# Kernel optimization log

Hardware: AMD Instinct MI355X
Metric: run time of the kernel (lower is better)

Reference implementation:

```python
import jax, jax.numpy as jnp
import numpy as np
import math

B, H, W = 16, 48, 48
D_MODEL, D_EXP, D_INNER, N, DR, K = 96, 192, 192, 16, 6, 4
L = H * W

def depthwise_conv(x, w, b, pad):
    # x: NHWC, w: (kh,kw,1,C) depthwise kernel
    C = x.shape[-1]
    y = jax.lax.conv_general_dilated(x, w, (1, 1), [(pad, pad), (pad, pad)],
        dimension_numbers=('NHWC', 'HWIO', 'NHWC'), feature_group_count=C)
    return y + b

def bn(x, g, be, m, v):
    return (x - m) * jax.lax.rsqrt(v + 1e-5) * g + be

def cross_scan(x):  # (B,C,H,W) -> (B,K,C,L): row-major, col-major, and their reverses
    x0 = x.reshape(B, -1, L)
    x1 = jnp.swapaxes(x, 2, 3).reshape(B, -1, L)
    return jnp.stack([x0, x1, x0[..., ::-1], x1[..., ::-1]], axis=1)

def cross_merge(ys):  # (B,K,C,L) -> (B,C,L)
    y0 = ys[:, 0] + ys[:, 2][..., ::-1]
    y1 = ys[:, 1] + ys[:, 3][..., ::-1]
    y1 = jnp.swapaxes(y1.reshape(B, -1, W, H), 2, 3).reshape(B, -1, L)
    return y0 + y1

def selective_scan(u, delta, A, Bm, Cm):
    # u, delta: (B,K,D,L); A: (K,D,N); Bm, Cm: (B,K,N,L)
    h0 = jnp.zeros((B, K, D_INNER, N), dtype=u.dtype)
    def step(h, inp):
        d_t, u_t, B_t, C_t = inp  # (B,K,D),(B,K,D),(B,K,N),(B,K,N)
        h = h * jnp.exp(d_t[..., None] * A) + (d_t * u_t)[..., None] * B_t[:, :, None, :]
        return h, jnp.einsum('bkdn,bkn->bkd', h, C_t)
    seq = (jnp.moveaxis(delta, -1, 0), jnp.moveaxis(u, -1, 0),
           jnp.moveaxis(Bm, -1, 0), jnp.moveaxis(Cm, -1, 0))
    _, ys = jax.lax.scan(step, h0, seq)
    return jnp.moveaxis(ys, 0, -1)  # (B,K,D,L)

def setup_inputs():
    key = jax.random.key(0)
    ks = jax.random.split(key, 30)
    rn = lambda i, s, sc=0.05: jax.random.normal(ks[i], s, jnp.float32) * sc
    # faithful dt bias init: inverse-softplus of delta ~ logU[1e-3, 1e-1]
    dlt = jnp.exp(jax.random.uniform(ks[0], (K, D_INNER)) * (math.log(0.1) - math.log(0.001)) + math.log(0.001))
    return {
        'x': jax.random.normal(ks[1], (B, H, W, D_MODEL), jnp.float32),
        'in_proj_w': rn(2, (2 * D_EXP, D_MODEL)),
        'conv_w': rn(3, (3, 3, 1, D_EXP), 0.2),
        'conv_b': rn(4, (D_EXP,)),
        'x_proj_w': rn(5, (K, DR + 2 * N, D_INNER)),
        'dt_proj_w': rn(6, (K, D_INNER, DR), DR ** -0.5),
        'dt_proj_b': dlt + jnp.log(-jnp.expm1(-dlt)),
        'A_log': jnp.tile(jnp.log(jnp.arange(1, N + 1, dtype=jnp.float32)), (K, D_INNER, 1)),
        'Ds': jnp.ones((K, D_INNER), jnp.float32),
        'out_proj_w': rn(7, (D_MODEL, D_EXP)),
        'e1_w': rn(8, (2 * D_EXP, D_EXP)), 'e1_b': rn(9, (2 * D_EXP,)),
        'bn1_g': jnp.ones((2 * D_EXP,), jnp.float32), 'bn1_b': rn(10, (2 * D_EXP,)),
        'bn1_m': rn(11, (2 * D_EXP,)), 'bn1_v': jnp.ones((2 * D_EXP,), jnp.float32),
        'e2_w': rn(12, (3, 3, 1, 2 * D_EXP), 0.2), 'e2_b': rn(13, (2 * D_EXP,)),
        'bn2_g': jnp.ones((2 * D_EXP,), jnp.float32), 'bn2_b': rn(14, (2 * D_EXP,)),
        'bn2_m': rn(15, (2 * D_EXP,)), 'bn2_v': jnp.ones((2 * D_EXP,), jnp.float32),
        'e3_w': rn(16, (D_EXP // 2, 2 * D_EXP)), 'e3_b': rn(17, (D_EXP // 2,)),
        'se1_w': rn(18, (D_EXP // 4, D_EXP // 2)), 'se1_b': rn(19, (D_EXP // 4,)),
        'se2_w': rn(20, (D_EXP // 2, D_EXP // 4)), 'se2_b': rn(21, (D_EXP // 2,)),
    }

def reference(x, in_proj_w, conv_w, conv_b, x_proj_w, dt_proj_w, dt_proj_b, A_log, Ds,
              out_proj_w, e1_w, e1_b, bn1_g, bn1_b, bn1_m, bn1_v, e2_w, e2_b,
              bn2_g, bn2_b, bn2_m, bn2_v, e3_w, e3_b, se1_w, se1_b, se2_w, se2_b):
    # in-projection -> (x, gate z)
    xz = jnp.einsum('bhwd,ed->bhwe', x, in_proj_w)
    xc, z = jnp.split(xz, 2, axis=-1)
    # depthwise conv + SiLU
    xc = jax.nn.silu(depthwise_conv(xc, conv_w, conv_b, 1))     # (B,H,W,C)
    xs = cross_scan(jnp.transpose(xc, (0, 3, 1, 2)))            # (B,K,C,L)
    # per-direction projections to (delta_rank, B, C)
    dbl = jnp.einsum('bkdl,kcd->bkcl', xs, x_proj_w)
    dts, Bm, Cm = dbl[:, :, :DR], dbl[:, :, DR:DR + N], dbl[:, :, DR + N:]
    delta = jax.nn.softplus(jnp.einsum('bkrl,kdr->bkdl', dts, dt_proj_w) + dt_proj_b[None, :, :, None])
    ys = selective_scan(xs, delta, -jnp.exp(A_log), Bm, Cm)
    ys = ys + Ds[None, :, :, None] * xs                          # D skip
    y = jnp.transpose(cross_merge(ys).reshape(B, -1, H, W), (0, 2, 3, 1))  # (B,H,W,C)
    y = y * jax.nn.silu(z)                                       # gate
    out = jnp.einsum('bhwe,de->bhwd', y, out_proj_w)
    # EFFN branch (1x1 -> BN/ReLU -> dw3x3 -> BN/ReLU -> 1x1 -> SE)
    t = jax.nn.relu(bn(jnp.einsum('bhwc,oc->bhwo', y, e1_w) + e1_b, bn1_g, bn1_b, bn1_m, bn1_v))
    t = jax.nn.relu(bn(depthwise_conv(t, e2_w, e2_b, 1), bn2_g, bn2_b, bn2_m, bn2_v))
    t = jnp.einsum('bhwc,oc->bhwo', t, e3_w) + e3_b              # (B,H,W,D_MODEL)
    s = jnp.mean(t, axis=(1, 2))
    s = jax.nn.sigmoid(jax.nn.relu(s @ se1_w.T + se1_b) @ se2_w.T + se2_b)
    return out + t * s[:, None, None, :]
```

## Files before the change

### kernel.cpp

```cpp
#include <hip/hip_runtime.h>
#include <cstddef>

#define BB   16
#define HH   48
#define WW   48
#define LL   2304
#define MTOT 36864
#define DM   96
#define DE   192
#define NS   16
#define KD   4
#define DRK  6
#define CPROJ 152
#define DSTRIDE 40
#define SCH  36
#define LC   64

typedef unsigned short u16;
typedef __attribute__((ext_vector_type(8))) short  short8;
typedef __attribute__((ext_vector_type(4))) float  f4;
typedef __attribute__((ext_vector_type(2))) float  f2;
typedef __attribute__((ext_vector_type(4))) unsigned short us4;

__device__ __forceinline__ float bf2f(u16 u) {
  union { unsigned int i; float f; } c; c.i = ((unsigned int)u) << 16; return c.f;
}
__device__ __forceinline__ u16 f2bf(float f) {
  union { float f; unsigned int i; } c; c.f = f;
  unsigned int r = c.i + 0x7FFFu + ((c.i >> 16) & 1u);
  return (u16)(r >> 16);
}

__global__ __launch_bounds__(256) void cast_f2b(
    const float* __restrict__ src, u16* __restrict__ dst, int n4)
{
  int i = blockIdx.x * 256 + threadIdx.x;
  if (i >= n4) return;
  float4 v = ((const float4*)src)[i];
  us4 o;
  o.x = f2bf(v.x); o.y = f2bf(v.y); o.z = f2bf(v.z); o.w = f2bf(v.w);
  ((us4*)dst)[i] = o;
}

__global__ __launch_bounds__(256) void cast_weights(
    const float* __restrict__ w0, const float* __restrict__ w1,
    const float* __restrict__ w2, const float* __restrict__ w3,
    const float* __restrict__ w4, u16* __restrict__ dst)
{
  int i = blockIdx.x * 256 + threadIdx.x;
  if (i >= 195072) return;
  float v;
  if      (i <  36864) v = w0[i];
  else if (i <  66048) v = w1[i - 36864];
  else if (i <  84480) v = w2[i - 66048];
  else if (i < 158208) v = w3[i - 84480];
  else                 v = w4[i - 158208];
  dst[i] = f2bf(v);
}

template<int MODE, int K>
__global__ __launch_bounds__(256) void gemm_mfma(
    const u16* __restrict__ A, const u16* __restrict__ Wb,
    float* __restrict__ outF, u16* __restrict__ outB,
    const float* __restrict__ q0, const float* __restrict__ q1,
    const float* __restrict__ q2, const float* __restrict__ q3,
    const float* __restrict__ q4, int N)
{
  constexpr int KP = K + 8;
  constexpr int KC = K / 8;
  __shared__ u16 Bs[64 * KP];

  const int tid = threadIdx.x;
  const int m0 = blockIdx.x * 256;
  const int n0 = blockIdx.y * 64;

  for (int i = tid; i < 64 * KC; i += 256) {
    int row = i / KC, ch = i - row * KC;
    short8 v = {0, 0, 0, 0, 0, 0, 0, 0};
    if (n0 + row < N)
      v = *(const short8*)(Wb + (size_t)(n0 + row) * K + ch * 8);
    *(short8*)(&Bs[row * KP + ch * 8]) = v;
  }
  __syncthreads();

  const int lane = tid & 63;
  const int wv = tid >> 6;
  const int l15 = lane & 15;
  const int q8 = (lane >> 4) << 3;

  f4 acc[4][4];
#pragma unroll
  for (int mi = 0; mi < 4; ++mi)
#pragma unroll
    for (int ni = 0; ni < 4; ++ni)
      acc[mi][ni] = (f4){0.f, 0.f, 0.f, 0.f};

  const u16* Ap = A + (size_t)(m0 + wv * 64 + l15) * K + q8;

  for (int k0 = 0; k0 < K; k0 += 32) {
    short8 af[4], bf[4];
#pragma unroll
    for (int mi = 0; mi < 4; ++mi)
      af[mi] = *(const short8*)(Ap + (size_t)(mi * 16) * K + k0);
#pragma unroll
    for (int ni = 0; ni < 4; ++ni)
      bf[ni] = *(const short8*)(&Bs[(ni * 16 + l15) * KP + k0 + q8]);
#pragma unroll
    for (int mi = 0; mi < 4; ++mi)
#pragma unroll
      for (int ni = 0; ni < 4; ++ni)
        acc[mi][ni] = __builtin_amdgcn_mfma_f32_16x16x32_bf16(
            af[mi], bf[ni], acc[mi][ni], 0, 0, 0);
  }

#pragma unroll
  for (int mi = 0; mi < 4; ++mi) {
    int rbase = m0 + wv * 64 + mi * 16 + ((lane >> 4) << 2);
#pragma unroll
    for (int ni = 0; ni < 4; ++ni) {
      int col = n0 + ni * 16 + l15;
#pragma unroll
      for (int r = 0; r < 4; ++r) {
        int row = rbase + r;
        float v = acc[mi][ni][r];
        if (MODE == 0) {
          if (col < DE) outB[(size_t)row * DE + col] = f2bf(v);
          else          outF[(size_t)row * DE + (col - DE)] = v / (1.f + __expf(-v));
        } else if (MODE == 1) {
          if (col < N) outF[(size_t)row * N + col] = v;
        } else if (MODE == 2) {
          float t = (v + q0[col] - q3[col]) * q1[col] * rsqrtf(q4[col] + 1e-5f) + q2[col];
          outB[(size_t)row * 384 + col] = f2bf(fmaxf(t, 0.f));
        } else if (MODE == 3) {
          if (col < N) outF[(size_t)row * N + col] = v + q0[col];
        } else {
          if (col < CPROJ) {
            int kk = col / 38, cc = col - kk * 38;
            outF[((size_t)kk * MTOT + row) * DSTRIDE + cc] = v;
          }
        }
      }
    }
  }
}

template<int MODE, int C>
__global__ __launch_bounds__(256) void dwconv_b(
    const u16* __restrict__ in, const float* __restrict__ w9,
    const float* __restrict__ bias,
    const float* __restrict__ bg, const float* __restrict__ bbe,
    const float* __restrict__ bm, const float* __restrict__ bv,
    u16* __restrict__ out)
{
  constexpr int C4 = C / 4;
  int idx = blockIdx.x * 256 + threadIdx.x;
  if (idx >= MTOT * C4) return;
  int c4 = idx % C4;
  int pos = idx / C4;
  int hw = pos % LL;
  int b = pos / LL;
  int h = hw / WW, w = hw - (hw / WW) * WW;
  int c = c4 * 4;
  f4 acc = (f4){0.f, 0.f, 0.f, 0.f};
#pragma unroll
  for (int dh = -1; dh <= 1; ++dh) {
    int h2 = h + dh;
    if ((unsigned)h2 >= (unsigned)HH) continue;
#pragma unroll
    for (int dw = -1; dw <= 1; ++dw) {
      int w2 = w + dw;
      if ((unsigned)w2 >= (unsigned)WW) continue;
      const u16* ip = in + ((size_t)(b * LL + h2 * WW + w2)) * C + c;
      us4 uv = *(const us4*)ip;
      float4 wvv = *(const float4*)(w9 + ((dh + 1) * 3 + (dw + 1)) * C + c);
      acc[0] = fmaf(bf2f(uv.x), wvv.x, acc[0]);
      acc[1] = fmaf(bf2f(uv.y), wvv.y, acc[1]);
      acc[2] = fmaf(bf2f(uv.z), wvv.z, acc[2]);
      acc[3] = fmaf(bf2f(uv.w), wvv.w, acc[3]);
    }
  }
  float4 bi = *(const float4*)(bias + c);
  float vv[4] = {acc[0] + bi.x, acc[1] + bi.y, acc[2] + bi.z, acc[3] + bi.w};
  us4 o;
  if (MODE == 0) {
#pragma unroll
    for (int j = 0; j < 4; ++j) vv[j] = vv[j] / (1.f + __expf(-vv[j]));
  } else {
    float4 g = *(const float4*)(bg + c);
    float4 be = *(const float4*)(bbe + c);
    float4 mm = *(const float4*)(bm + c);
    float4 va = *(const float4*)(bv + c);
    float gg[4] = {g.x, g.y, g.z, g.w}, bb[4] = {be.x, be.y, be.z, be.w};
    float m4[4] = {mm.x, mm.y, mm.z, mm.w}, v4[4] = {va.x, va.y, va.z, va.w};
#pragma unroll
    for (int j = 0; j < 4; ++j)
      vv[j] = fmaxf((vv[j] - m4[j]) * gg[j] * rsqrtf(v4[j] + 1e-5f) + bb[j], 0.f);
  }
  o.x = f2bf(vv[0]); o.y = f2bf(vv[1]); o.z = f2bf(vv[2]); o.w = f2bf(vv[3]);
  *(us4*)(out + (size_t)pos * C + c) = o;
}

struct PosIter {
  int k, pos, hq, wq;
  __device__ __forceinline__ void init(int kk, int i0) {
    k = kk;
    if (k == 0) { pos = i0; }
    else if (k == 2) { pos = LL - 1 - i0; }
    else {
      int j = (k == 1) ? i0 : (LL - 1 - i0);
      wq = j / HH; hq = j - wq * HH;
      pos = hq * WW + wq;
    }
  }
  __device__ __forceinline__ void next() {
    if (k == 0) { ++pos; }
    else if (k == 2) { --pos; }
    else if (k == 1) {
      ++hq; pos += WW;
      if (hq == HH) { hq = 0; ++wq; pos = wq; }
    } else {
      --hq; pos -= WW;
      if (hq < 0) { hq = HH - 1; --wq; pos = hq * WW + wq; }
    }
  }
};

__global__ __launch_bounds__(192) void scan_part1(
    const u16* __restrict__ xc, const float* __restrict__ dbl,
    const float* __restrict__ dtw, const float* __restrict__ dtb,
    const float* __restrict__ Alog,
    float* __restrict__ hloc, float* __restrict__ sd)
{
  int blk = blockIdx.x;
  int s = blk % SCH;
  int bk = blk / SCH;
  int k = bk & 3;
  int b = bk >> 2;
  int d = threadIdx.x;
  float wr[DRK];
#pragma unroll
  for (int r = 0; r < DRK; ++r) wr[r] = dtw[(k * DE + d) * DRK + r];
  float bias = dtb[k * DE + d];
  float a0 = -__expf(Alog[(k * DE + d) * NS]);
  f2 h2[8];
#pragma unroll
  for (int j = 0; j < 8; ++j) h2[j] = (f2){0.f, 0.f};
  float sumd = 0.f;
  const u16* xcb = xc + (size_t)b * LL * DE + d;
  const float* dpr = dbl + ((size_t)k * MTOT + (size_t)b * LL) * DSTRIDE;
  PosIter it; it.init(k, s * LC);
#pragma unroll 1
  for (int ii = 0; ii < LC; ++ii) {
    const float4* dp4 = (const float4*)(dpr + (size_t)it.pos * DSTRIDE);
    float4 rr[6];
#pragma unroll
    for (int t = 0; t < 6; ++t) rr[t] = dp4[t];
    const float* rf = (const float*)rr;
    float g = bias;
#pragma unroll
    for (int r = 0; r < DRK; ++r) g = fmaf(rf[r], wr[r], g);
    float e = __expf(g);
    float delta = (g > 20.f) ? g : __logf(1.f + e);
    float p = __expf(delta * a0);
    sumd += delta;
    float du = delta * bf2f(xcb[(size_t)it.pos * DE]);
    f2 du2 = (f2){du, du};
    f2 qq = (f2){p, p * p};
    f2 p2 = (f2){qq.y, qq.y};
#pragma unroll
    for (int j = 0; j < 8; ++j) {
      f2 bv = (f2){rf[6 + 2 * j], rf[7 + 2 * j]};
      h2[j] = h2[j] * qq + du2 * bv;
      qq = qq * p2;
    }
    it.next();
  }
  size_t base = ((size_t)blk * NS) * DE + d;
#pragma unroll
  for (int j = 0; j < 8; ++j) {
    hloc[base + (size_t)(2 * j) * DE] = h2[j].x;
    hloc[base + (size_t)(2 * j + 1) * DE] = h2[j].y;
  }
  sd[(size_t)blk * DE + d] = sumd;
}

__global__ __launch_bounds__(192) void scan_part2(
    const float* __restrict__ hloc, const float* __restrict__ sd,
    const float* __restrict__ Alog, float* __restrict__ hin)
{
  int bk = blockIdx.x;
  int k = bk & 3;
  int d = threadIdx.x;
  float a0 = -__expf(Alog[(k * DE + d) * NS]);
  float h[NS];
#pragma unroll
  for (int n = 0; n < NS; ++n) h[n] = 0.f;
  for (int s = 0; s < SCH; ++s) {
    size_t base = ((size_t)(bk * SCH + s) * NS) * DE + d;
#pragma unroll
    for (int n = 0; n < NS; ++n) hin[base + (size_t)n * DE] = h[n];
    float qs = __expf(sd[(size_t)(bk * SCH + s) * DE + d] * a0);
    float q = 1.f;
#pragma unroll
    for (int n = 0; n < NS; ++n) {
      q *= qs;
      h[n] = fmaf(h[n], q, hloc[base + (size_t)n * DE]);
    }
  }
}

__global__ __launch_bounds__(192) void scan_part3(
    const u16* __restrict__ xc, const float* __restrict__ dbl,
    const float* __restrict__ dtw, const float* __restrict__ dtb,
    const float* __restrict__ Alog, const float* __restrict__ Dsw,
    const float* __restrict__ hin, float* __restrict__ ym)
{
  int blk = blockIdx.x;
  int s = blk % SCH;
  int bk = blk / SCH;
  int k = bk & 3;
  int b = bk >> 2;
  int d = threadIdx.x;
  float wr[DRK];
#pragma unroll
  for (int r = 0; r < DRK; ++r) wr[r] = dtw[(k * DE + d) * DRK + r];
  float bias = dtb[k * DE + d];
  float a0 = -__expf(Alog[(k * DE + d) * NS]);
  float dsv = Dsw[k * DE + d];
  f2 h2[8];
  size_t hbase = ((size_t)blk * NS) * DE + d;
#pragma unroll
  for (int j = 0; j < 8; ++j) {
    h2[j].x = hin[hbase + (size_t)(2 * j) * DE];
    h2[j].y = hin[hbase + (size_t)(2 * j + 1) * DE];
  }
  const u16* xcb = xc + (size_t)b * LL * DE + d;
  const float* dpr = dbl + ((size_t)k * MTOT + (size_t)b * LL) * DSTRIDE;
  float* ymb = ym + (size_t)b * LL * DE + d;
  PosIter it; it.init(k, s * LC);
#pragma unroll 1
  for (int ii = 0; ii < LC; ++ii) {
    const float4* dp4 = (const float4*)(dpr + (size_t)it.pos * DSTRIDE);
    float4 rr[10];
#pragma unroll
    for (int t = 0; t < 10; ++t) rr[t] = dp4[t];
    const float* rf = (const float*)rr;
    float g = bias;
#pragma unroll
    for (int r = 0; r < DRK; ++r) g = fmaf(rf[r], wr[r], g);
    float e = __expf(g);
    float delta = (g > 20.f) ? g : __logf(1.f + e);
    float p = __expf(delta * a0);
    float u = bf2f(xcb[(size_t)it.pos * DE]);
    float du = delta * u;
    f2 du2 = (f2){du, du};
    f2 qq = (f2){p, p * p};
    f2 p2 = (f2){qq.y, qq.y};
    f2 y2 = (f2){0.f, 0.f};
#pragma unroll
    for (int j = 0; j < 8; ++j) {
      f2 bv = (f2){rf[6 + 2 * j], rf[7 + 2 * j]};
      f2 cv = (f2){rf[22 + 2 * j], rf[23 + 2 * j]};
      h2[j] = h2[j] * qq + du2 * bv;
      y2 = y2 + h2[j] * cv;
      qq = qq * p2;
    }
    float y = fmaf(dsv, u, y2.x + y2.y);
    atomicAdd(&ymb[(size_t)it.pos * DE], y);
    it.next();
  }
}

__global__ __launch_bounds__(256) void ymul_k(
    const float* __restrict__ ym, const float* __restrict__ sz, u16* __restrict__ y)
{
  int i4 = blockIdx.x * 256 + threadIdx.x;
  if (i4 >= (MTOT * DE / 4)) return;
  float4 a = ((const float4*)ym)[i4];
  float4 z = ((const float4*)sz)[i4];
  us4 r;
  r.x = f2bf(a.x * z.x); r.y = f2bf(a.y * z.y);
  r.z = f2bf(a.z * z.z); r.w = f2bf(a.w * z.w);
  ((us4*)y)[i4] = r;
}

__global__ __launch_bounds__(384) void se_reduce(
    const float* __restrict__ t3, float* __restrict__ smean)
{
  __shared__ float red[384];
  int b = blockIdx.x, ch = blockIdx.y;
  int t = threadIdx.x;
  int o = t % 96, g = t / 96;
  float acc = 0.f;
  int base = b * LL + ch * 256;
  for (int r = g; r < 256; r += 4)
    acc += t3[(size_t)(base + r) * 96 + o];
  red[t] = acc;
  __syncthreads();
  if (t < 96)
    atomicAdd(&smean[b * 96 + t], red[t] + red[t + 96] + red[t + 192] + red[t + 288]);
}

__global__ __launch_bounds__(256) void se_mlp(
    const float* __restrict__ smean, const float* __restrict__ w1, const float* __restrict__ b1,
    const float* __restrict__ w2, const float* __restrict__ b2, float* __restrict__ s)
{
  __shared__ float s1[16 * 48];
  const float scl = 1.f / (float)LL;
  int t = threadIdx.x;
  for (int idx = t; idx < 16 * 48; idx += 256) {
    int b = idx / 48, j = idx % 48;
    float dot = 0.f;
    for (int i = 0; i < 96; ++i) dot = fmaf(smean[b * 96 + i], w1[j * 96 + i], dot);
    s1[idx] = fmaxf(fmaf(dot, scl, b1[j]), 0.f);
  }
  __syncthreads();
  for (int idx = t; idx < 16 * 96; idx += 256) {
    int b = idx / 96, o = idx % 96;
    float acc = b2[o];
    for (int j = 0; j < 48; ++j) acc = fmaf(s1[b * 48 + j], w2[o * 48 + j], acc);
    s[idx] = 1.f / (1.f + __expf(-acc));
  }
}

__global__ __launch_bounds__(256) void final_k(
    const float* __restrict__ o1, const float* __restrict__ t3,
    const float* __restrict__ s, float* __restrict__ out)
{
  int i4 = blockIdx.x * 256 + threadIdx.x;
  if (i4 >= (MTOT * 96 / 4)) return;
  int i = i4 * 4;
  int b = i / (LL * 96);
  int o = i % 96;
  float4 a = ((const float4*)o1)[i4];
  float4 c = ((const float4*)t3)[i4];
  const float* sp = s + b * 96 + o;
  float4 r;
  r.x = a.x + c.x * sp[0];
  r.y = a.y + c.y * sp[1];
  r.z = a.z + c.z * sp[2];
  r.w = a.w + c.w * sp[3];
  ((float4*)out)[i4] = r;
}

extern "C" void kernel_launch(void* const* d_in, const int* in_sizes, int n_in,
                              void* d_out, int out_size, void* d_ws, size_t ws_size,
                              hipStream_t stream) {
  (void)in_sizes; (void)n_in; (void)out_size;
  const float* x          = (const float*)d_in[0];
  const float* in_proj_w  = (const float*)d_in[1];
  const float* conv_w     = (const float*)d_in[2];
  const float* conv_b     = (const float*)d_in[3];
  const float* x_proj_w   = (const float*)d_in[4];
  const float* dt_proj_w  = (const float*)d_in[5];
  const float* dt_proj_b  = (const float*)d_in[6];
  const float* A_log      = (const float*)d_in[7];
  const float* Ds         = (const float*)d_in[8];
  const float* out_proj_w = (const float*)d_in[9];
  const float* e1_w       = (const float*)d_in[10];
  const float* e1_b       = (const float*)d_in[11];
  const float* bn1_g      = (const float*)d_in[12];
  const float* bn1_b      = (const float*)d_in[13];
  const float* bn1_m      = (const float*)d_in[14];
  const float* bn1_v      = (const float*)d_in[15];
  const float* e2_w       = (const float*)d_in[16];
  const float* e2_b       = (const float*)d_in[17];
  const float* bn2_g      = (const float*)d_in[18];
  const float* bn2_b      = (const float*)d_in[19];
  const float* bn2_m      = (const float*)d_in[20];
  const float* bn2_v      = (const float*)d_in[21];
  const float* e3_w       = (const float*)d_in[22];
  const float* e3_b       = (const float*)d_in[23];
  const float* se1_w      = (const float*)d_in[24];
  const float* se1_b      = (const float*)d_in[25];
  const float* se2_w      = (const float*)d_in[26];
  const float* se2_b      = (const float*)d_in[27];

  char* ws = (char*)d_ws;
  const size_t A0 = 0;
  const size_t B0 = 28311552;
  const size_t C0 = 56623104;
  const size_t E0 = 84934656;
  const size_t F0 = E0 + (size_t)KD * MTOT * DSTRIDE * 4;
  const size_t G0 = F0 + 28311552;
  const size_t Gsd    = G0 + 14155776;
  const size_t Gwcat  = Gsd + 1769472;
  const size_t Gsmean = Gwcat + 390144;
  const size_t Gsbuf  = Gsmean + 6144;
  const size_t need   = Gsbuf + 6144;
  if (ws_size < need) return;

  u16*   xw     = (u16*)(ws + A0);
  float* hin    = (float*)(ws + A0);
  float* o1     = (float*)(ws + A0);
  float* t3     = (float*)(ws + A0 + 14155776);
  u16*   xcraw  = (u16*)(ws + B0);
  float* hloc   = (float*)(ws + B0);
  u16*   yb     = (u16*)(ws + B0);
  u16*   t2b    = (u16*)(ws + B0);
  float* szb    = (float*)(ws + C0);
  u16*   t1b    = (u16*)(ws + C0);
  float* dblb   = (float*)(ws + E0);
  float* ymrg   = (float*)(ws + F0);
  u16*   xcb    = (u16*)(ws + G0);
  float* sdb    = (float*)(ws + Gsd);
  u16*   wcat   = (u16*)(ws + Gwcat);
  float* smean  = (float*)(ws + Gsmean);
  float* sbuf   = (float*)(ws + Gsbuf);

  hipMemsetAsync(ymrg, 0, 28311552, stream);
  hipMemsetAsync(smean, 0, 6144, stream);

  hipLaunchKernelGGL(cast_f2b, dim3((MTOT * DM / 4 + 255) / 256), dim3(256), 0, stream,
                     x, xw, MTOT * DM / 4);
  hipLaunchKernelGGL(cast_weights, dim3((195072 + 255) / 256), dim3(256), 0, stream,
                     in_proj_w, x_proj_w, out_proj_w, e1_w, e3_w, wcat);

  hipLaunchKernelGGL((gemm_mfma<0, 96>), dim3(MTOT / 256, 6), dim3(256), 0, stream,
                     xw, wcat + 0, szb, xcraw,
                     nullptr, nullptr, nullptr, nullptr, nullptr, 384);
  hipLaunchKernelGGL((dwconv_b<0, DE>), dim3((MTOT * (DE / 4) + 255) / 256), dim3(256), 0, stream,
                     xcraw, conv_w, conv_b, nullptr, nullptr, nullptr, nullptr, xcb);
  hipLaunchKernelGGL((gemm_mfma<4, 192>), dim3(MTOT / 256, 3), dim3(256), 0, stream,
                     xcb, wcat + 36864, dblb, nullptr,
                     nullptr, nullptr, nullptr, nullptr, nullptr, CPROJ);
  hipLaunchKernelGGL(scan_part1, dim3(BB * KD * SCH), dim3(DE), 0, stream,
                     xcb, dblb, dt_proj_w, dt_proj_b, A_log, hloc, sdb);
  hipLaunchKernelGGL(scan_part2, dim3(BB * KD), dim3(DE), 0, stream,
                     hloc, sdb, A_log, hin);
  hipLaunchKernelGGL(scan_part3, dim3(BB * KD * SCH), dim3(DE), 0, stream,
                     xcb, dblb, dt_proj_w, dt_proj_b, A_log, Ds, hin, ymrg);
  hipLaunchKernelGGL(ymul_k, dim3((MTOT * DE / 4 + 255) / 256), dim3(256), 0, stream,
                     ymrg, szb, yb);
  hipLaunchKernelGGL((gemm_mfma<1, 192>), dim3(MTOT / 256, 2), dim3(256), 0, stream,
                     yb, wcat + 66048, o1, nullptr,
                     nullptr, nullptr, nullptr, nullptr, nullptr, 96);
  hipLaunchKernelGGL((gemm_mfma<2, 192>), dim3(MTOT / 256, 6), dim3(256), 0, stream,
                     yb, wcat + 84480, nullptr, t1b,
                     e1_b, bn1_g, bn1_b, bn1_m, bn1_v, 384);
  hipLaunchKernelGGL((dwconv_b<1, 384>), dim3((MTOT * 96 + 255) / 256), dim3(256), 0, stream,
                     t1b, e2_w, e2_b, bn2_g, bn2_b, bn2_m, bn2_v, t2b);
  hipLaunchKernelGGL((gemm_mfma<3, 384>), dim3(MTOT / 256, 2), dim3(256), 0, stream,
                     t2b, wcat + 158208, t3, nullptr,
                     e3_b, nullptr, nullptr, nullptr, nullptr, 96);
  hipLaunchKernelGGL(se_reduce, dim3(BB, 9), dim3(384), 0, stream, t3, smean);
  hipLaunchKernelGGL(se_mlp, dim3(1), dim3(256), 0, stream,
                     smean, se1_w, se1_b, se2_w, se2_b, sbuf);
  hipLaunchKernelGGL(final_k, dim3((MTOT * 96 / 4 + 255) / 256), dim3(256), 0, stream,
                     o1, t3, sbuf, (float*)d_out);
}
```

Measured before the change: 515.6 us.

## Pack scan B/C in bf16, store gate in bf16, pair directions to drop atomics

The x_proj output row is shrunk from 40 floats to 24 by storing the dt-rank values as fp32 and B/C as packed bf16. The silu gate is likewise stored as bf16. scan_part3 now has each block handle a direction and its reverse over mirrored chunks, applying the gate inline and writing plain stores into two per-parity buffers. This replaces float atomicAdds into a zeroed buffer. A new ysum kernel adds the two buffers, and the memset and the separate gate-multiply kernel are removed. The costs are lower B/C and gate precision, half as many scan_part3 blocks each doing twice the serial work, and one extra full fp32 buffer read.

```diff
diff --git a/kernel.cpp b/kernel.cpp
--- a/kernel.cpp
+++ b/kernel.cpp
@@ -12,7 +12,7 @@
 #define KD   4
 #define DRK  6
 #define CPROJ 152
-#define DSTRIDE 40
+#define DROW 24
 #define SCH  36
 #define LC   64
 
@@ -29,6 +29,11 @@
   union { float f; unsigned int i; } c; c.f = f;
   unsigned int r = c.i + 0x7FFFu + ((c.i >> 16) & 1u);
   return (u16)(r >> 16);
+}
+__device__ __forceinline__ f2 bfpair(unsigned int w) {
+  union { unsigned int i; float f; } lo, hi;
+  lo.i = w << 16; hi.i = w & 0xFFFF0000u;
+  return (f2){lo.f, hi.f};
 }
 
 __global__ __launch_bounds__(256) void cast_f2b(
@@ -125,7 +130,7 @@
         float v = acc[mi][ni][r];
         if (MODE == 0) {
           if (col < DE) outB[(size_t)row * DE + col] = f2bf(v);
-          else          outF[(size_t)row * DE + (col - DE)] = v / (1.f + __expf(-v));
+          else ((u16*)outF)[(size_t)row * DE + (col - DE)] = f2bf(v / (1.f + __expf(-v)));
         } else if (MODE == 1) {
           if (col < N) outF[(size_t)row * N + col] = v;
         } else if (MODE == 2) {
@@ -136,7 +141,9 @@
         } else {
           if (col < CPROJ) {
             int kk = col / 38, cc = col - kk * 38;
-            outF[((size_t)kk * MTOT + row) * DSTRIDE + cc] = v;
+            float* rowp = outF + ((size_t)kk * MTOT + row) * DROW;
+            if (cc < 6) rowp[cc] = v;
+            else ((u16*)(rowp + 6))[cc - 6] = f2bf(v);
           }
         }
       }
@@ -225,6 +232,7 @@
   }
 };
 
+
 __global__ __launch_bounds__(192) void scan_part1(
     const u16* __restrict__ xc, const float* __restrict__ dbl,
     const float* __restrict__ dtw, const float* __restrict__ dtb,
@@ -247,15 +255,16 @@
   for (int j = 0; j < 8; ++j) h2[j] = (f2){0.f, 0.f};
   float sumd = 0.f;
   const u16* xcb = xc + (size_t)b * LL * DE + d;
-  const float* dpr = dbl + ((size_t)k * MTOT + (size_t)b * LL) * DSTRIDE;
+  const float* dpr = dbl + ((size_t)k * MTOT + (size_t)b * LL) * DROW;
   PosIter it; it.init(k, s * LC);
 #pragma unroll 1
   for (int ii = 0; ii < LC; ++ii) {
-    const float4* dp4 = (const float4*)(dpr + (size_t)it.pos * DSTRIDE);
+    const float4* dp4 = (const float4*)(dpr + (size_t)it.pos * DROW);
     float4 rr[6];
 #pragma unroll
     for (int t = 0; t < 6; ++t) rr[t] = dp4[t];
     const float* rf = (const float*)rr;
+    const unsigned int* bw = ((const unsigned int*)rr) + 6;
     float g = bias;
 #pragma unroll
     for (int r = 0; r < DRK; ++r) g = fmaf(rf[r], wr[r], g);
@@ -269,7 +278,7 @@
     f2 p2 = (f2){qq.y, qq.y};
 #pragma unroll
     for (int j = 0; j < 8; ++j) {
-      f2 bv = (f2){rf[6 + 2 * j], rf[7 + 2 * j]};
+      f2 bv = bfpair(bw[j]);
       h2[j] = h2[j] * qq + du2 * bv;
       qq = qq * p2;
     }
@@ -313,74 +322,86 @@
     const u16* __restrict__ xc, const float* __restrict__ dbl,
     const float* __restrict__ dtw, const float* __restrict__ dtb,
     const float* __restrict__ Alog, const float* __restrict__ Dsw,
-    const float* __restrict__ hin, float* __restrict__ ym)
+    const float* __restrict__ hin, const u16* __restrict__ gate,
+    float* __restrict__ yA, float* __restrict__ yB)
 {
   int blk = blockIdx.x;
-  int s = blk % SCH;
-  int bk = blk / SCH;
-  int k = bk & 3;
-  int b = bk >> 2;
+  int w = blk % SCH;
+  int t = blk / SCH;
+  int dp = t & 1;
+  int b = t >> 1;
   int d = threadIdx.x;
-  float wr[DRK];
-#pragma unroll
-  for (int r = 0; r < DRK; ++r) wr[r] = dtw[(k * DE + d) * DRK + r];
-  float bias = dtb[k * DE + d];
-  float a0 = -__expf(Alog[(k * DE + d) * NS]);
-  float dsv = Dsw[k * DE + d];
-  f2 h2[8];
-  size_t hbase = ((size_t)blk * NS) * DE + d;
-#pragma unroll
-  for (int j = 0; j < 8; ++j) {
-    h2[j].x = hin[hbase + (size_t)(2 * j) * DE];
-    h2[j].y = hin[hbase + (size_t)(2 * j + 1) * DE];
-  }
+  float* yrow = (dp ? yB : yA) + (size_t)b * LL * DE + d;
   const u16* xcb = xc + (size_t)b * LL * DE + d;
-  const float* dpr = dbl + ((size_t)k * MTOT + (size_t)b * LL) * DSTRIDE;
-  float* ymb = ym + (size_t)b * LL * DE + d;
-  PosIter it; it.init(k, s * LC);
+  const u16* gb  = gate + (size_t)b * LL * DE + d;
+
 #pragma unroll 1
-  for (int ii = 0; ii < LC; ++ii) {
-    const float4* dp4 = (const float4*)(dpr + (size_t)it.pos * DSTRIDE);
-    float4 rr[10];
-#pragma unroll
-    for (int t = 0; t < 10; ++t) rr[t] = dp4[t];
-    const float* rf = (const float*)rr;
-    float g = bias;
-#pragma unroll
-    for (int r = 0; r < DRK; ++r) g = fmaf(rf[r], wr[r], g);
-    float e = __expf(g);
-    float delta = (g > 20.f) ? g : __logf(1.f + e);
-    float p = __expf(delta * a0);
-    float u = bf2f(xcb[(size_t)it.pos * DE]);
-    float du = delta * u;
-    f2 du2 = (f2){du, du};
-    f2 qq = (f2){p, p * p};
-    f2 p2 = (f2){qq.y, qq.y};
-    f2 y2 = (f2){0.f, 0.f};
+  for (int pass = 0; pass < 2; ++pass) {
+    int k = dp + 2 * pass;
+    int c = pass ? (SCH - 1 - w) : w;
+    float wr[DRK];
+#pragma unroll
+    for (int r = 0; r < DRK; ++r) wr[r] = dtw[(k * DE + d) * DRK + r];
+    float bias = dtb[k * DE + d];
+    float a0 = -__expf(Alog[(k * DE + d) * NS]);
+    float dsv = Dsw[k * DE + d];
+    f2 h2[8];
+    size_t hbase = (((size_t)(b * KD + k) * SCH + c) * NS) * DE + d;
 #pragma unroll
     for (int j = 0; j < 8; ++j) {
-      f2 bv = (f2){rf[6 + 2 * j], rf[7 + 2 * j]};
-      f2 cv = (f2){rf[22 + 2 * j], rf[23 + 2 * j]};
-      h2[j] = h2[j] * qq + du2 * bv;
-      y2 = y2 + h2[j] * cv;
-      qq = qq * p2;
-    }
-    float y = fmaf(dsv, u, y2.x + y2.y);
-    atomicAdd(&ymb[(size_t)it.pos * DE], y);
-    it.next();
-  }
-}
-
-__global__ __launch_bounds__(256) void ymul_k(
-    const float* __restrict__ ym, const float* __restrict__ sz, u16* __restrict__ y)
+      h2[j].x = hin[hbase + (size_t)(2 * j) * DE];
+      h2[j].y = hin[hbase + (size_t)(2 * j + 1) * DE];
+    }
+    const float* dpr = dbl + ((size_t)k * MTOT + (size_t)b * LL) * DROW;
+    PosIter it; it.init(k, c * LC);
+#pragma unroll 1
+    for (int ii = 0; ii < LC; ++ii) {
+      const float4* dp4 = (const float4*)(dpr + (size_t)it.pos * DROW);
+      float4 rr[6];
+#pragma unroll
+      for (int tt = 0; tt < 6; ++tt) rr[tt] = dp4[tt];
+      const float* rf = (const float*)rr;
+      const unsigned int* bw = ((const unsigned int*)rr) + 6;
+      const unsigned int* cw = ((const unsigned int*)rr) + 14;
+      float g = bias;
+#pragma unroll
+      for (int r = 0; r < DRK; ++r) g = fmaf(rf[r], wr[r], g);
+      float e = __expf(g);
+      float delta = (g > 20.f) ? g : __logf(1.f + e);
+      float p = __expf(delta * a0);
+      float u = bf2f(xcb[(size_t)it.pos * DE]);
+      float du = delta * u;
+      f2 du2 = (f2){du, du};
+      f2 qq = (f2){p, p * p};
+      f2 p2 = (f2){qq.y, qq.y};
+      f2 y2 = (f2){0.f, 0.f};
+#pragma unroll
+      for (int j = 0; j < 8; ++j) {
+        f2 bv = bfpair(bw[j]);
+        f2 cv = bfpair(cw[j]);
+        h2[j] = h2[j] * qq + du2 * bv;
+        y2 = y2 + h2[j] * cv;
+        qq = qq * p2;
+      }
+      float y = fmaf(dsv, u, y2.x + y2.y);
+      float out = y * bf2f(gb[(size_t)it.pos * DE]);
+      if (pass) out += yrow[(size_t)it.pos * DE];
+      yrow[(size_t)it.pos * DE] = out;
+      it.next();
+    }
+  }
+}
+
+__global__ __launch_bounds__(256) void ysum_k(
+    const float* __restrict__ yA, const float* __restrict__ yB, u16* __restrict__ y)
 {
   int i4 = blockIdx.x * 256 + threadIdx.x;
   if (i4 >= (MTOT * DE / 4)) return;
-  float4 a = ((const float4*)ym)[i4];
-  float4 z = ((const float4*)sz)[i4];
+  float4 a = ((const float4*)yA)[i4];
+  float4 bq = ((const float4*)yB)[i4];
   us4 r;
-  r.x = f2bf(a.x * z.x); r.y = f2bf(a.y * z.y);
-  r.z = f2bf(a.z * z.z); r.w = f2bf(a.w * z.w);
+  r.x = f2bf(a.x + bq.x); r.y = f2bf(a.y + bq.y);
+  r.z = f2bf(a.z + bq.z); r.w = f2bf(a.w + bq.w);
   ((us4*)y)[i4] = r;
 }
 
@@ -477,38 +498,39 @@
   const float* se2_b      = (const float*)d_in[27];
 
   char* ws = (char*)d_ws;
-  const size_t A0 = 0;
-  const size_t B0 = 28311552;
-  const size_t C0 = 56623104;
-  const size_t E0 = 84934656;
-  const size_t F0 = E0 + (size_t)KD * MTOT * DSTRIDE * 4;
-  const size_t G0 = F0 + 28311552;
-  const size_t Gsd    = G0 + 14155776;
-  const size_t Gwcat  = Gsd + 1769472;
-  const size_t Gsmean = Gwcat + 390144;
+  const size_t S1 = 0;
+  const size_t S2 = 28311552;
+  const size_t S3 = 56623104;
+  const size_t S4 = 70778880;
+  const size_t S5 = 84934656;
+  const size_t S6 = 99090432;
+  const size_t S6b = S6 + 28311552;
+  const size_t S7 = 155713536;
+  const size_t S8 = S7 + 1769472;
+  const size_t Gsmean = S8 + 390144;
   const size_t Gsbuf  = Gsmean + 6144;
   const size_t need   = Gsbuf + 6144;
   if (ws_size < need) return;
 
-  u16*   xw     = (u16*)(ws + A0);
-  float* hin    = (float*)(ws + A0);
-  float* o1     = (float*)(ws + A0);
-  float* t3     = (float*)(ws + A0 + 14155776);
-  u16*   xcraw  = (u16*)(ws + B0);
-  float* hloc   = (float*)(ws + B0);
-  u16*   yb     = (u16*)(ws + B0);
-  u16*   t2b    = (u16*)(ws + B0);
-  float* szb    = (float*)(ws + C0);
-  u16*   t1b    = (u16*)(ws + C0);
-  float* dblb   = (float*)(ws + E0);
-  float* ymrg   = (float*)(ws + F0);
-  u16*   xcb    = (u16*)(ws + G0);
-  float* sdb    = (float*)(ws + Gsd);
-  u16*   wcat   = (u16*)(ws + Gwcat);
+  u16*   xw     = (u16*)(ws + S1);
+  float* hloc   = (float*)(ws + S1);
+  u16*   yb     = (u16*)(ws + S1);
+  float* o1     = (float*)(ws + S1 + 14155776);
+  u16*   xcraw  = (u16*)(ws + S2);
+  float* hin    = (float*)(ws + S2);
+  u16*   t1b    = (u16*)(ws + S2);
+  u16*   szb    = (u16*)(ws + S3);
+  float* t3     = (float*)(ws + S3);
+  u16*   xcb    = (u16*)(ws + S4);
+  float* dblb   = (float*)(ws + S5);
+  float* yA     = (float*)(ws + S6);
+  float* yB     = (float*)(ws + S6b);
+  u16*   t2b    = (u16*)(ws + S6);
+  float* sdb    = (float*)(ws + S7);
+  u16*   wcat   = (u16*)(ws + S8);
   float* smean  = (float*)(ws + Gsmean);
   float* sbuf   = (float*)(ws + Gsbuf);
 
-  hipMemsetAsync(ymrg, 0, 28311552, stream);
   hipMemsetAsync(smean, 0, 6144, stream);
 
   hipLaunchKernelGGL(cast_f2b, dim3((MTOT * DM / 4 + 255) / 256), dim3(256), 0, stream,
@@ -517,7 +539,7 @@
                      in_proj_w, x_proj_w, out_proj_w, e1_w, e3_w, wcat);
 
   hipLaunchKernelGGL((gemm_mfma<0, 96>), dim3(MTOT / 256, 6), dim3(256), 0, stream,
-                     xw, wcat + 0, szb, xcraw,
+                     xw, wcat + 0, (float*)szb, xcraw,
                      nullptr, nullptr, nullptr, nullptr, nullptr, 384);
   hipLaunchKernelGGL((dwconv_b<0, DE>), dim3((MTOT * (DE / 4) + 255) / 256), dim3(256), 0, stream,
                      xcraw, conv_w, conv_b, nullptr, nullptr, nullptr, nullptr, xcb);
@@ -528,10 +550,10 @@
                      xcb, dblb, dt_proj_w, dt_proj_b, A_log, hloc, sdb);
   hipLaunchKernelGGL(scan_part2, dim3(BB * KD), dim3(DE), 0, stream,
                      hloc, sdb, A_log, hin);
-  hipLaunchKernelGGL(scan_part3, dim3(BB * KD * SCH), dim3(DE), 0, stream,
-                     xcb, dblb, dt_proj_w, dt_proj_b, A_log, Ds, hin, ymrg);
-  hipLaunchKernelGGL(ymul_k, dim3((MTOT * DE / 4 + 255) / 256), dim3(256), 0, stream,
-                     ymrg, szb, yb);
+  hipLaunchKernelGGL(scan_part3, dim3(BB * 2 * SCH), dim3(DE), 0, stream,
+                     xcb, dblb, dt_proj_w, dt_proj_b, A_log, Ds, hin, szb, yA, yB);
+  hipLaunchKernelGGL(ysum_k, dim3((MTOT * DE / 4 + 255) / 256), dim3(256), 0, stream,
+                     yA, yB, yb);
   hipLaunchKernelGGL((gemm_mfma<1, 192>), dim3(MTOT / 256, 2), dim3(256), 0, stream,
                      yb, wcat + 66048, o1, nullptr,
                      nullptr, nullptr, nullptr, nullptr, nullptr, 96);
```

Result: slower. 530.2 us (+2.8%).
